# Performance work log

Measured on AMD Instinct MI355X. Metric: run time of the kernel, lower is better.

## Reference

```python
import jax, jax.numpy as jnp
import numpy as np

K = 5
BASE_LAMBDA = 0.05
BASE_DELTA = 0.01
ITERS = 3
STEP = 0.2
FUSION_SCALE = 2.0
EPS = 1e-8


def _param_sets():
    # Deterministic (jitter_strength=0) version of SASConfig._generate_param_sets.
    # View 0 is identity; views 1..K-1 get linearly spaced lambda and coupled delta.
    lmin, lmax = BASE_LAMBDA * 0.5, BASE_LAMBDA * 1.5
    lams, deltas = [], []
    for i in range(K - 1):
        lam = lmin + (lmax - lmin) * i / max(1, K - 2)
        lams.append(lam)
        deltas.append(BASE_DELTA * np.sqrt(lam / (BASE_LAMBDA + 1e-8)))
    return jnp.asarray(lams, jnp.float32), jnp.asarray(deltas, jnp.float32)


def _huber_tv(x, lam, delta):
    # Anisotropic Huber-TV diffusion, skip_clamp=True (artifact denoising path).
    # x: [B,C,H,W]
    xd = x
    for _ in range(ITERS):
        dx = jnp.pad(xd[:, :, :, 1:] - xd[:, :, :, :-1], ((0, 0), (0, 0), (0, 0), (0, 1)))
        dy = jnp.pad(xd[:, :, 1:, :] - xd[:, :, :-1, :], ((0, 0), (0, 0), (0, 1), (0, 0)))
        gx = dx / (delta + jnp.abs(dx))
        gy = dy / (delta + jnp.abs(dy))
        # divergence with replicated first element (div[...,0] = g[...,0])
        div_x = gx - jnp.pad(gx[:, :, :, :-1], ((0, 0), (0, 0), (0, 0), (1, 0)))
        div_y = gy - jnp.pad(gy[:, :, :-1, :], ((0, 0), (0, 0), (1, 0), (0, 0)))
        xd = xd - STEP * (xd - x - lam * (div_x + div_y))
    return xd


def setup_inputs() -> dict:
    key = jax.random.key(0)
    x = jax.random.normal(key, (32, 3, 256, 256), dtype=jnp.float32)
    return {"x": x}


def reference(x):
    B = x.shape[0]
    # torch.median over flattened |artifact| (lower median for even count)
    flat = jnp.abs(x).reshape(B, -1)
    n = flat.shape[1]
    scale = jnp.sort(flat, axis=1)[:, (n - 1) // 2].reshape(B, 1, 1, 1) + 1e-8

    lams, deltas = _param_sets()
    xn = x / scale
    denoised = jax.vmap(lambda l, d: _huber_tv(xn, l, d))(lams, deltas)  # [K-1,B,C,H,W]
    arts = jnp.concatenate([x[None], denoised * scale[None]], axis=0)  # [K,B,C,H,W]

    # Robust MAD-weighted fusion (K=5 is odd, jnp.median == torch.median over dim 0)
    med = jnp.median(arts, axis=0)
    dev = jnp.abs(arts - med[None])
    mad = jnp.median(dev, axis=0)
    mad = jnp.maximum(mad, 0.1 * mad.mean())
    w = jnp.exp(-dev / (FUSION_SCALE * mad[None]))
    fused = (w * arts).sum(axis=0) / (w.sum(axis=0) + EPS)
    return fused
```

## Files before the change

### kernel.cpp

```cpp
#include <hip/hip_runtime.h>
#include <math.h>

typedef unsigned int u32;
typedef unsigned long long u64;
typedef float v2f __attribute__((ext_vector_type(2)));

#define NPIX 6291456


__device__ __forceinline__ float med3f(float a, float b, float c) {
    return fmaxf(fminf(a, b), fminf(fmaxf(a, b), c));
}
__device__ __forceinline__ float med5f(float a0, float a1, float a2, float a3, float a4) {
    float mn01 = fminf(a0, a1), mx01 = fmaxf(a0, a1);
    float mn34 = fminf(a3, a4), mx34 = fmaxf(a3, a4);
    return med3f(a2, fmaxf(mn01, mn34), fminf(mx01, mx34));
}
__device__ __forceinline__ u32 packbf(float lo, float hi) {
    u32 a = __float_as_uint(lo), b = __float_as_uint(hi);
    a = (a + 0x7FFFu + ((a >> 16) & 1u)) >> 16;
    b = (b + 0x7FFFu + ((b >> 16) & 1u)) >> 16;
    return a | (b << 16);
}

__device__ __forceinline__ u32 scan1024(u32 v, u32* wtot) {
    int lane = threadIdx.x & 63, wid = threadIdx.x >> 6;
    u32 inc = v;
    #pragma unroll
    for (int off = 1; off < 64; off <<= 1) {
        u32 o = __shfl_up(inc, off);
        if (lane >= off) inc += o;
    }
    __syncthreads();
    if (lane == 63) wtot[wid] = inc;
    __syncthreads();
    for (int w = 0; w < wid; ++w) inc += wtot[w];
    return inc;
}


__global__ __launch_bounds__(1024) void hist_kernel(
        const float* __restrict__ x, u32* __restrict__ hist,
        float* __restrict__ madsum) {
    __shared__ u32 lh[16400];
    int b = blockIdx.x >> 3, s = blockIdx.x & 7, t = threadIdx.x;
    uint4 z = make_uint4(0u, 0u, 0u, 0u);
    #pragma unroll
    for (int j = 0; j < 4; ++j) ((uint4*)lh)[t + j * 1024] = z;
    if (t < 4) ((uint4*)lh)[4096 + t] = z;
    __syncthreads();
    const float4* xb = (const float4*)(x + (size_t)b * 196608 + s * 24576);
    u32 sub = (u32)(t & 3) * 4100u;
    #pragma unroll
    for (int i = 0; i < 6; ++i) {
        float4 v = xb[t + i * 1024];
        atomicAdd(&lh[sub + (__float_as_uint(fabsf(v.x)) >> 19)], 1u);
        atomicAdd(&lh[sub + (__float_as_uint(fabsf(v.y)) >> 19)], 1u);
        atomicAdd(&lh[sub + (__float_as_uint(fabsf(v.z)) >> 19)], 1u);
        atomicAdd(&lh[sub + (__float_as_uint(fabsf(v.w)) >> 19)], 1u);
    }
    __syncthreads();
    u32 a0 = 0, a1 = 0, a2 = 0, a3 = 0;
    #pragma unroll
    for (int sb = 0; sb < 4; ++sb) {
        uint4 hv = *(const uint4*)&lh[sb * 4100u + (u32)t * 4u];
        a0 += hv.x; a1 += hv.y; a2 += hv.z; a3 += hv.w;
    }
    u32* hb = hist + ((size_t)b * 8 + s) * 4096;
    ((uint4*)hb)[t] = make_uint4(a0, a1, a2, a3);
    if (s == 0 && t == 0 && b == 0) *madsum = 0.0f;
}


__global__ __launch_bounds__(1024) void extract_kernel(
        const float* __restrict__ x, const u32* __restrict__ hist,
        u32* __restrict__ members, u32* __restrict__ scount,
        u32* __restrict__ selBin, u32* __restrict__ selKr) {
    __shared__ u32 sbuf[8192];
    __shared__ u32 wtot[16];
    __shared__ u32 sBin, lcnt;
    int b = blockIdx.x >> 3, s = blockIdx.x & 7, t = threadIdx.x, lane = t & 63;
    if (t == 0) lcnt = 0u;
    const u32* hb = hist + (size_t)b * 32768;
    u32 s4[4] = {0u, 0u, 0u, 0u};
    #pragma unroll
    for (int sl = 0; sl < 8; ++sl) {
        uint4 h4 = ((const uint4*)(hb + sl * 4096))[t];
        s4[0] += h4.x; s4[1] += h4.y; s4[2] += h4.z; s4[3] += h4.w;
    }
    u32 sum = s4[0] + s4[1] + s4[2] + s4[3];
    u32 inc = scan1024(sum, wtot);
    u32 exc = inc - sum;
    u32 k = 98303u;
    if (exc <= k && k < inc) {
        u32 kr = k - exc;
        int j = 0;
        while (kr >= s4[j]) { kr -= s4[j]; ++j; }
        sBin = (u32)(t * 4 + j);
        if (s == 0) { selBin[b] = (u32)(t * 4 + j); selKr[b] = kr; }
    }
    __syncthreads();
    u32 bin = sBin;
    const float4* xb = (const float4*)(x + (size_t)b * 196608 + s * 24576);
    #pragma unroll 2
    for (int i = 0; i < 6; ++i) {
        float4 v = xb[t + i * 1024];
        float vv[4] = {v.x, v.y, v.z, v.w};
        #pragma unroll
        for (int e = 0; e < 4; ++e) {
            u32 bits = __float_as_uint(fabsf(vv[e]));
            bool is = (bits >> 19) == bin;
            u64 ball = __ballot(is);
            if (ball) {
                u32 cnt = (u32)__popcll(ball);
                u32 base = 0;
                if (lane == 0) base = atomicAdd(&lcnt, cnt);
                base = __shfl(base, 0);
                if (is) {
                    u32 p = base + (u32)__popcll(ball & ((1ull << lane) - 1ull));
                    if (p < 8192u) sbuf[p] = bits & 0x7FFFFu;
                }
            }
        }
    }
    __syncthreads();
    u32 cnt = lcnt; if (cnt > 8192u) cnt = 8192u;
    u32* mb = members + ((size_t)b * 8 + s) * 8192;
    for (u32 i = (u32)t; i < cnt; i += 1024u) mb[i] = sbuf[i];
    if (t == 0) scount[b * 8 + s] = cnt;
}


__global__ __launch_bounds__(1024) void select_kernel(
        const u32* __restrict__ scount, const u32* __restrict__ members,
        const u32* __restrict__ selBin, const u32* __restrict__ selKr,
        float* __restrict__ scale) {
    __shared__ u32 sbuf[8192];
    __shared__ u32 h[128];
    __shared__ u32 wtot[16];
    __shared__ u32 sPfx, sK;
    int b = blockIdx.x, t = threadIdx.x;
    u32 c[8], off[8], tot = 0u;
    #pragma unroll
    for (int s = 0; s < 8; ++s) {
        c[s] = scount[b * 8 + s];
        off[s] = tot;
        tot += c[s];
    }
    #pragma unroll
    for (int s = 0; s < 8; ++s) {
        const u32* mb = members + ((size_t)b * 8 + s) * 8192;
        for (u32 i = (u32)t; i < c[s]; i += 1024u) {
            u32 p = off[s] + i;
            if (p < 8192u) sbuf[p] = mb[i];
        }
    }
    u32 m = tot; if (m > 8192u) m = 8192u;
    if (t == 0) { sPfx = 0u; sK = selKr[b]; }
    __syncthreads();
    const int shf[3] = {12, 6, 0};
    const int wd[3]  = {7, 6, 6};
    const u32 msk[3] = {127u, 63u, 63u};
    #pragma unroll 1
    for (int rd = 0; rd < 3; ++rd) {
        u32 pfx = sPfx, k2 = sK;
        if (t < 128) h[t] = 0u;
        __syncthreads();
        for (u32 i = (u32)t; i < m; i += 1024u) {
            u32 v = sbuf[i];
            if ((v >> (shf[rd] + wd[rd])) == pfx)
                atomicAdd(&h[(v >> shf[rd]) & msk[rd]], 1u);
        }
        __syncthreads();
        u32 nb = msk[rd] + 1u;
        u32 cc = ((u32)t < nb) ? h[t] : 0u;
        u32 inc2 = scan1024(cc, wtot);
        u32 exc2 = inc2 - cc;
        if ((u32)t < nb && exc2 <= k2 && k2 < inc2) {
            sPfx = (pfx << wd[rd]) | (u32)t;
            sK = k2 - exc2;
        }
        __syncthreads();
    }
    if (t == 0)
        scale[b] = __uint_as_float((selBin[b] << 19) | sPfx) + 1e-8f;
}


__device__ __forceinline__ float dpp_shl1(float v) {
    return __uint_as_float((u32)__builtin_amdgcn_update_dpp(
        0, (int)__float_as_uint(v), 0x130, 0xF, 0xF, true));
}
__device__ __forceinline__ float dpp_shr1(float v) {
    return __uint_as_float((u32)__builtin_amdgcn_update_dpp(
        0, (int)__float_as_uint(v), 0x138, 0xF, 0xF, true));
}

__device__ __forceinline__ v2f hub2(v2f d, float del) {
    v2f den = __builtin_elementwise_abs(d) + (v2f){del, del};
    v2f r;
    r.x = __builtin_amdgcn_rcpf(den.x);
    r.y = __builtin_amdgcn_rcpf(den.y);
    return d * r;
}
__device__ __forceinline__ v2f upd2(v2f b, v2f xn, v2f dv, float lam) {
    v2f t = __builtin_elementwise_fma((v2f){-lam, -lam}, dv, b - xn);
    return __builtin_elementwise_fma((v2f){-0.2f, -0.2f}, t, b);
}

__device__ __forceinline__ float4 stage4(float4 B, float4 C, float4 xn, float4& gyp,
                                         int row, float mR3, float mL0,
                                         float lam, float del) {
    float mr = (row < 255) ? 1.f : 0.f;
    float m0 = (row == 0) ? 0.f : 1.f;
    v2f Bl = {B.x, B.y}, Bh = {B.z, B.w};
    v2f mr2 = {mr, mr}, m02 = {m0, m0};
    v2f gyl = hub2((v2f){C.x, C.y} - Bl, del) * mr2;
    v2f gyh = hub2((v2f){C.z, C.w} - Bh, del) * mr2;
    v2f dvl = gyl - (v2f){gyp.x, gyp.y} * m02;
    v2f dvh = gyh - (v2f){gyp.z, gyp.w} * m02;
    gyp.x = gyl.x; gyp.y = gyl.y; gyp.z = gyh.x; gyp.w = gyh.y;
    float B0n = dpp_shl1(B.x);
    v2f gl = hub2((v2f){B.y, B.z} - Bl, del);
    v2f gh = hub2((v2f){B.w, B0n} - Bh, del) * (v2f){1.f, mR3};
    float gp = dpp_shr1(gh.y) * mL0;
    v2f totl = (gl - (v2f){gp, gl.x}) + dvl;
    v2f toth = (gh - (v2f){gl.y, gh.x}) + dvh;
    v2f ol = upd2(Bl, (v2f){xn.x, xn.y}, totl, lam);
    v2f oh = upd2(Bh, (v2f){xn.z, xn.w}, toth, lam);
    float4 o;
    o.x = ol.x; o.y = ol.y; o.z = oh.x; o.w = oh.y;
    return o;
}

__global__ __launch_bounds__(256, 6) void denoise_kernel(
        const float* __restrict__ x, const float* __restrict__ scale,
        u32* __restrict__ arts, float* __restrict__ madsum,
        float4 lam4, float4 del4) {
    __shared__ float sex[2][5][256];
    __shared__ float red[4];
    int t = threadIdx.x, lane = t & 63, wid = t >> 6;
    int img = blockIdx.x >> 3;
    int seg = blockIdx.x & 7;
    float sc = scale[img / 3];
    float lam = ((wid == 0) ? lam4.x : (wid == 1) ? lam4.y : (wid == 2) ? lam4.z : lam4.w) * sc;
    float del = ((wid == 0) ? del4.x : (wid == 1) ? del4.y : (wid == 2) ? del4.z : del4.w) * sc;
    float mR3 = (lane == 63) ? 0.f : 1.f;
    float mL0 = (lane == 0) ? 0.f : 1.f;
    const float4* xp = (const float4*)(x + (size_t)img * 65536) + lane;
    u32* ap = arts + (size_t)wid * (NPIX / 2) + (size_t)img * 32768 + lane * 2;

    float4 z4 = {0.f, 0.f, 0.f, 0.f};
    float4 cur1 = z4, cur2 = z4, gyp1 = z4, gyp2 = z4, gyp3 = z4;
    float4 n0 = z4, n1 = z4, n2 = z4;
    int out_lo = seg * 32, out_hi = out_lo + 31;
    int rs = (out_lo >= 3) ? out_lo - 3 : 0;
    int rend = out_hi + 3;
    float msum = 0.f;

    float4 nl = xp[rs << 6];
    for (int r = rs; r <= rend; ++r) {
        int rn = (r + 1 <= 255) ? r + 1 : 255;
        float4 nxt = xp[rn << 6];
        int r1 = r - 1, r2 = r - 2, r3 = r - 3;
        float4 x1 = stage4(n0,   nl, n0, gyp1, r1, mR3, mL0, lam, del);
        float4 x2 = stage4(cur1, x1, n1, gyp2, r2, mR3, mL0, lam, del);
        float4 x3 = stage4(cur2, x2, n2, gyp3, r3, mR3, mL0, lam, del);
        cur1 = x1; cur2 = x2;
        if (r3 >= out_lo) {
            uint2 pk;
            pk.x = packbf(x3.x, x3.y);
            pk.y = packbf(x3.z, x3.w);
            *(uint2*)(ap + (r3 << 7)) = pk;
            int pb = r3 & 1;
            *(float4*)&sex[pb][wid + 1][lane * 4] = x3;
            if (wid == 0) *(float4*)&sex[pb][0][lane * 4] = n2;
            __syncthreads();
            int c = wid * 64 + lane;
            float a0 = sex[pb][0][c], a1 = sex[pb][1][c], a2 = sex[pb][2][c],
                  a3 = sex[pb][3][c], a4 = sex[pb][4][c];
            float med = med5f(a0, a1, a2, a3, a4);
            msum += med5f(fabsf(a0 - med), fabsf(a1 - med), fabsf(a2 - med),
                          fabsf(a3 - med), fabsf(a4 - med));
        }
        n2 = n1; n1 = n0; n0 = nl;
        nl = nxt;
    }
    #pragma unroll
    for (int off = 32; off > 0; off >>= 1) msum += __shfl_down(msum, off);
    if (lane == 0) red[wid] = msum;
    __syncthreads();
    if (t == 0) atomicAdd(madsum, red[0] + red[1] + red[2] + red[3]);
}


__global__ __launch_bounds__(256) void fuse_kernel(
        const float* __restrict__ x, const u32* __restrict__ artsU,
        const float* __restrict__ madsum, float* __restrict__ out) {
    int t = blockIdx.x * 256 + threadIdx.x;
    float floorv = 0.1f * (*madsum) * (1.0f / 6291456.0f);
    float4 xv = ((const float4*)x)[t];
    uint2 q0 = ((const uint2*)(artsU))[t];
    uint2 q1 = ((const uint2*)(artsU + NPIX / 2))[t];
    uint2 q2 = ((const uint2*)(artsU + NPIX))[t];
    uint2 q3 = ((const uint2*)(artsU + 3 * (NPIX / 2)))[t];
    float4 o;
#define FUSE1(res, A0, U0, U1, U2, U3, SH) { \
        float a0 = A0; \
        float a1 = __uint_as_float(SH(U0)), a2 = __uint_as_float(SH(U1)); \
        float a3 = __uint_as_float(SH(U2)), a4 = __uint_as_float(SH(U3)); \
        float med = med5f(a0, a1, a2, a3, a4); \
        float d0 = fabsf(a0 - med), d1 = fabsf(a1 - med), d2 = fabsf(a2 - med); \
        float d3 = fabsf(a3 - med), d4 = fabsf(a4 - med); \
        float mad = med5f(d0, d1, d2, d3, d4); \
        float mm = fmaxf(mad, floorv); \
        float inv = 0.5f / mm; \
        float w0 = __expf(-d0 * inv), w1 = __expf(-d1 * inv), w2 = __expf(-d2 * inv); \
        float w3 = __expf(-d3 * inv), w4 = __expf(-d4 * inv); \
        float swt = w0 + w1 + w2 + w3 + w4; \
        float sva = fmaf(w0, a0, fmaf(w1, a1, fmaf(w2, a2, fmaf(w3, a3, w4 * a4)))); \
        res = sva / (swt + 1e-8f); \
    }
#define LO16(u) ((u) << 16)
#define HI16(u) ((u) & 0xFFFF0000u)
    FUSE1(o.x, xv.x, q0.x, q1.x, q2.x, q3.x, LO16);
    FUSE1(o.y, xv.y, q0.x, q1.x, q2.x, q3.x, HI16);
    FUSE1(o.z, xv.z, q0.y, q1.y, q2.y, q3.y, LO16);
    FUSE1(o.w, xv.w, q0.y, q1.y, q2.y, q3.y, HI16);
#undef FUSE1
#undef LO16
#undef HI16
    ((float4*)out)[t] = o;
}


extern "C" void kernel_launch(void* const* d_in, const int* in_sizes, int n_in,
                              void* d_out, int out_size, void* d_ws, size_t ws_size,
                              hipStream_t stream) {
    const float* x = (const float*)d_in[0];
    float* out = (float*)d_out;
    char* ws = (char*)d_ws;
    float* scale  = (float*)ws;
    float* madsum = (float*)(ws + 128);
    u32* selBin   = (u32*)(ws + 384);
    u32* selKr    = (u32*)(ws + 512);
    u32* artsU    = (u32*)(ws + 1024);
    u32* hist     = artsU;
    u32* members  = artsU + (size_t)32 * 8 * 4096;
    u32* scount   = members + (size_t)32 * 8 * 8192;

    hist_kernel<<<256, 1024, 0, stream>>>(x, hist, madsum);
    extract_kernel<<<256, 1024, 0, stream>>>(x, hist, members, scount, selBin, selKr);
    select_kernel<<<32, 1024, 0, stream>>>(scount, members, selBin, selKr, scale);

    float lamf[4], delf[4];
    for (int i = 0; i < 4; ++i) {
        double lam = 0.025 + 0.05 * (double)i / 3.0;
        lamf[i] = (float)lam;
        delf[i] = (float)(0.01 * sqrt(lam / (0.05 + 1e-8)));
    }
    float4 lam4 = make_float4(lamf[0], lamf[1], lamf[2], lamf[3]);
    float4 del4 = make_float4(delf[0], delf[1], delf[2], delf[3]);

    denoise_kernel<<<768, 256, 0, stream>>>(x, scale, artsU, madsum, lam4, del4);
    fuse_kernel<<<6144, 256, 0, stream>>>(x, artsU, madsum, out);
}
```

Before: 170.6 us.

## Fuse median extraction and selection into one per-image kernel with scan compaction

Replaces the 256-block extract kernel and the 32-block select kernel with a single 32-block kernel. Each block counts in-bin elements, uses a block scan to compute deterministic per-thread output offsets, compacts them into shared memory, and runs the radix refinement. This removes a launch, the members/scount global round trip and the shared atomics. In exchange, each block reads its whole image twice with only 32 blocks, which greatly reduces parallelism for the memory pass.

```diff
diff --git a/kernel.cpp b/kernel.cpp
--- a/kernel.cpp
+++ b/kernel.cpp
@@ -72,15 +72,14 @@
 }
 
 
-__global__ __launch_bounds__(1024) void extract_kernel(
+__global__ __launch_bounds__(1024) void binext_kernel(
         const float* __restrict__ x, const u32* __restrict__ hist,
-        u32* __restrict__ members, u32* __restrict__ scount,
-        u32* __restrict__ selBin, u32* __restrict__ selKr) {
+        float* __restrict__ scale) {
     __shared__ u32 sbuf[8192];
+    __shared__ u32 h[128];
     __shared__ u32 wtot[16];
-    __shared__ u32 sBin, lcnt;
-    int b = blockIdx.x >> 3, s = blockIdx.x & 7, t = threadIdx.x, lane = t & 63;
-    if (t == 0) lcnt = 0u;
+    __shared__ u32 sBin, sKr, sTot, sPfx, sK;
+    int b = blockIdx.x, t = threadIdx.x;
     const u32* hb = hist + (size_t)b * 32768;
     u32 s4[4] = {0u, 0u, 0u, 0u};
     #pragma unroll
@@ -97,67 +96,40 @@
         int j = 0;
         while (kr >= s4[j]) { kr -= s4[j]; ++j; }
         sBin = (u32)(t * 4 + j);
-        if (s == 0) { selBin[b] = (u32)(t * 4 + j); selKr[b] = kr; }
+        sKr = kr;
     }
     __syncthreads();
     u32 bin = sBin;
-    const float4* xb = (const float4*)(x + (size_t)b * 196608 + s * 24576);
+    const float4* xb = (const float4*)(x + (size_t)b * 196608);
+    u32 m = 0u;
+    #pragma unroll 4
+    for (int i = 0; i < 48; ++i) {
+        float4 v = xb[t + i * 1024];
+        m += ((__float_as_uint(fabsf(v.x)) >> 19) == bin);
+        m += ((__float_as_uint(fabsf(v.y)) >> 19) == bin);
+        m += ((__float_as_uint(fabsf(v.z)) >> 19) == bin);
+        m += ((__float_as_uint(fabsf(v.w)) >> 19) == bin);
+    }
+    u32 minc = scan1024(m, wtot);
+    u32 mexc = minc - m;
+    if (t == 1023) sTot = minc;
+    u32 pos = mexc;
     #pragma unroll 2
-    for (int i = 0; i < 6; ++i) {
+    for (int i = 0; i < 48; ++i) {
         float4 v = xb[t + i * 1024];
         float vv[4] = {v.x, v.y, v.z, v.w};
         #pragma unroll
         for (int e = 0; e < 4; ++e) {
             u32 bits = __float_as_uint(fabsf(vv[e]));
-            bool is = (bits >> 19) == bin;
-            u64 ball = __ballot(is);
-            if (ball) {
-                u32 cnt = (u32)__popcll(ball);
-                u32 base = 0;
-                if (lane == 0) base = atomicAdd(&lcnt, cnt);
-                base = __shfl(base, 0);
-                if (is) {
-                    u32 p = base + (u32)__popcll(ball & ((1ull << lane) - 1ull));
-                    if (p < 8192u) sbuf[p] = bits & 0x7FFFFu;
-                }
+            if ((bits >> 19) == bin) {
+                if (pos < 8192u) sbuf[pos] = bits & 0x7FFFFu;
+                ++pos;
             }
         }
     }
-    __syncthreads();
-    u32 cnt = lcnt; if (cnt > 8192u) cnt = 8192u;
-    u32* mb = members + ((size_t)b * 8 + s) * 8192;
-    for (u32 i = (u32)t; i < cnt; i += 1024u) mb[i] = sbuf[i];
-    if (t == 0) scount[b * 8 + s] = cnt;
-}
-
-
-__global__ __launch_bounds__(1024) void select_kernel(
-        const u32* __restrict__ scount, const u32* __restrict__ members,
-        const u32* __restrict__ selBin, const u32* __restrict__ selKr,
-        float* __restrict__ scale) {
-    __shared__ u32 sbuf[8192];
-    __shared__ u32 h[128];
-    __shared__ u32 wtot[16];
-    __shared__ u32 sPfx, sK;
-    int b = blockIdx.x, t = threadIdx.x;
-    u32 c[8], off[8], tot = 0u;
-    #pragma unroll
-    for (int s = 0; s < 8; ++s) {
-        c[s] = scount[b * 8 + s];
-        off[s] = tot;
-        tot += c[s];
-    }
-    #pragma unroll
-    for (int s = 0; s < 8; ++s) {
-        const u32* mb = members + ((size_t)b * 8 + s) * 8192;
-        for (u32 i = (u32)t; i < c[s]; i += 1024u) {
-            u32 p = off[s] + i;
-            if (p < 8192u) sbuf[p] = mb[i];
-        }
-    }
-    u32 m = tot; if (m > 8192u) m = 8192u;
-    if (t == 0) { sPfx = 0u; sK = selKr[b]; }
-    __syncthreads();
+    if (t == 0) { sPfx = 0u; sK = sKr; }
+    __syncthreads();
+    u32 mm = sTot; if (mm > 8192u) mm = 8192u;
     const int shf[3] = {12, 6, 0};
     const int wd[3]  = {7, 6, 6};
     const u32 msk[3] = {127u, 63u, 63u};
@@ -166,7 +138,7 @@
         u32 pfx = sPfx, k2 = sK;
         if (t < 128) h[t] = 0u;
         __syncthreads();
-        for (u32 i = (u32)t; i < m; i += 1024u) {
+        for (u32 i = (u32)t; i < mm; i += 1024u) {
             u32 v = sbuf[i];
             if ((v >> (shf[rd] + wd[rd])) == pfx)
                 atomicAdd(&h[(v >> shf[rd]) & msk[rd]], 1u);
@@ -183,7 +155,7 @@
         __syncthreads();
     }
     if (t == 0)
-        scale[b] = __uint_as_float((selBin[b] << 19) | sPfx) + 1e-8f;
+        scale[b] = __uint_as_float((bin << 19) | sPfx) + 1e-8f;
 }
 
 
@@ -342,16 +314,11 @@
     char* ws = (char*)d_ws;
     float* scale  = (float*)ws;
     float* madsum = (float*)(ws + 128);
-    u32* selBin   = (u32*)(ws + 384);
-    u32* selKr    = (u32*)(ws + 512);
     u32* artsU    = (u32*)(ws + 1024);
     u32* hist     = artsU;
-    u32* members  = artsU + (size_t)32 * 8 * 4096;
-    u32* scount   = members + (size_t)32 * 8 * 8192;
 
     hist_kernel<<<256, 1024, 0, stream>>>(x, hist, madsum);
-    extract_kernel<<<256, 1024, 0, stream>>>(x, hist, members, scount, selBin, selKr);
-    select_kernel<<<32, 1024, 0, stream>>>(scount, members, selBin, selKr, scale);
+    binext_kernel<<<32, 1024, 0, stream>>>(x, hist, scale);
 
     float lamf[4], delf[4];
     for (int i = 0; i < 4; ++i) {
```

New measurement: 178.4 us. 4.6% more time.
